# Kernel optimization log

Hardware: AMD Instinct MI355X
Metric: run time of the kernel (lower is better)

## Reference

```python
import jax, jax.numpy as jnp
import numpy as np

B, N, DIM = 2, 2048, 512
H, DH = 8, 64            # heads, dim_head; inner_dim = H*DH = 512 == DIM -> to_out is Identity
BAND = 128               # mask keeps -128 <= j-i <= 127
LN_EPS = 1e-5


def _band_mask(n):
    i = jnp.arange(n)
    d = i[None, :] - i[:, None]          # j - i
    return (d >= -BAND) & (d < BAND)     # [n, n] bool


def setup_inputs() -> dict:
    key = jax.random.key(0)
    k1, k2 = jax.random.split(key, 2)
    x = jax.random.normal(k1, (B, N, DIM), dtype=jnp.float32)
    w_qkv = jax.random.normal(k2, (DIM, 3 * H * DH), dtype=jnp.float32) * (DIM ** -0.5)
    gamma = jnp.ones((DIM,), dtype=jnp.float32)
    beta = jnp.zeros((DIM,), dtype=jnp.float32)
    return {"x": x, "w_qkv": w_qkv, "gamma": gamma, "beta": beta}


def reference(x, w_qkv, gamma, beta):
    # LayerNorm
    mu = jnp.mean(x, axis=-1, keepdims=True)
    var = jnp.mean((x - mu) ** 2, axis=-1, keepdims=True)
    xn = (x - mu) * jax.lax.rsqrt(var + LN_EPS) * gamma + beta

    # qkv projection (no bias); split and reshape to [B, H, N, DH]
    qkv = xn @ w_qkv                                   # [B, N, 3*H*DH]
    q, k, v = jnp.split(qkv, 3, axis=-1)
    to_heads = lambda t: t.reshape(B, N, H, DH).transpose(0, 2, 1, 3)
    q, k, v = to_heads(q), to_heads(k), to_heads(v)

    # NOTE: original forward never applies self.scale -> no scaling here (faithful).
    attn = jnp.einsum('bhnd,bhmd->bhnm', q, k)         # [B, H, N, N]
    attn = jnp.where(_band_mask(N), attn, jnp.float32(-10000.0))
    probs = jax.nn.softmax(attn, axis=-1)
    out = jnp.einsum('bhnm,bhmd->bhnd', probs, v)      # [B, H, N, DH]
    out = out.transpose(0, 2, 1, 3).reshape(B, N, H * DH)
    return out  # to_out is Identity since inner_dim == dim
```

## Files before the change

kernel.cpp:

```cpp
#include <hip/hip_runtime.h>
#include <hip/hip_bf16.h>

#define B_    2
#define N_    2048
#define DIM_  512
#define H_    8
#define DH_   64
#define QKVW  1536
#define BAND_ 128
#define LN_EPS 1e-5f

typedef __attribute__((ext_vector_type(8))) short bf16x8;
typedef __attribute__((ext_vector_type(4))) float f32x4;
typedef __attribute__((ext_vector_type(8))) unsigned short ushort8;

__device__ __forceinline__ float bf2f(unsigned short u) {
    union { unsigned int i; float f; } w; w.i = ((unsigned int)u) << 16; return w.f;
}
__device__ __forceinline__ unsigned short f2bf(float f) {
    __hip_bfloat16 h = __float2bfloat16(f);
    return *reinterpret_cast<unsigned short*>(&h);
}
__device__ __forceinline__ void async_copy16(void* lds, const void* g) {
    __builtin_amdgcn_global_load_lds(
        (const __attribute__((address_space(1))) unsigned int*)g,
        (__attribute__((address_space(3))) unsigned int*)lds, 16, 0, 0);
}

__global__ __launch_bounds__(256) void prep_kernel(const float* __restrict__ x,
                                                   const float* __restrict__ gamma,
                                                   const float* __restrict__ beta,
                                                   const float* __restrict__ W,
                                                   unsigned short* __restrict__ xh,
                                                   unsigned short* __restrict__ xl,
                                                   unsigned short* __restrict__ Bh,
                                                   unsigned short* __restrict__ Bl) {
    __shared__ float T[64][65];
    if (blockIdx.x < 1024) {
        const int row  = blockIdx.x * 4 + (threadIdx.x >> 6);
        const int lane = threadIdx.x & 63;
        const float* xr = x + (size_t)row * DIM_ + lane * 8;
        float4 a = *(const float4*)xr;
        float4 c = *(const float4*)(xr + 4);
        float s  = (a.x + a.y) + (a.z + a.w) + (c.x + c.y) + (c.z + c.w);
        float sq = a.x*a.x + a.y*a.y + a.z*a.z + a.w*a.w
                 + c.x*c.x + c.y*c.y + c.z*c.z + c.w*c.w;
        #pragma unroll
        for (int o = 32; o; o >>= 1) { s += __shfl_xor(s, o); sq += __shfl_xor(sq, o); }
        const float mu  = s * (1.0f / DIM_);
        const float var = sq * (1.0f / DIM_) - mu * mu;
        const float rs  = rsqrtf(var + LN_EPS);
        float4 g0 = *(const float4*)(gamma + lane * 8);
        float4 g1 = *(const float4*)(gamma + lane * 8 + 4);
        float4 b0 = *(const float4*)(beta  + lane * 8);
        float4 b1 = *(const float4*)(beta  + lane * 8 + 4);
        const float fv[8] = {
            (a.x - mu) * rs * g0.x + b0.x, (a.y - mu) * rs * g0.y + b0.y,
            (a.z - mu) * rs * g0.z + b0.z, (a.w - mu) * rs * g0.w + b0.w,
            (c.x - mu) * rs * g1.x + b1.x, (c.y - mu) * rs * g1.y + b1.y,
            (c.z - mu) * rs * g1.z + b1.z, (c.w - mu) * rs * g1.w + b1.w };
        ushort8 h, l;
        #pragma unroll
        for (int j = 0; j < 8; ++j) {
            const unsigned short hv = f2bf(fv[j]);
            h[j] = hv; l[j] = f2bf(fv[j] - bf2f(hv));
        }
        *(ushort8*)(xh + (size_t)row * DIM_ + lane * 8) = h;
        *(ushort8*)(xl + (size_t)row * DIM_ + lane * 8) = l;
    } else {
        const int bx = blockIdx.x - 1024;
        const int n0 = (bx % 24) * 64, k0 = (bx / 24) * 64;
        const int tid = threadIdx.x;
        #pragma unroll
        for (int e = 0; e < 4; ++e) {
            const int lin = e * 256 + tid;
            const int kk = lin >> 4;
            const int n4 = (lin & 15) * 4;
            float4 f = *(const float4*)(W + (size_t)(k0 + kk) * QKVW + n0 + n4);
            T[kk][n4 + 0] = f.x; T[kk][n4 + 1] = f.y;
            T[kk][n4 + 2] = f.z; T[kk][n4 + 3] = f.w;
        }
        __syncthreads();
        #pragma unroll
        for (int e = 0; e < 4; ++e) {
            const int lin = e * 256 + tid;
            const int nn = lin >> 4;
            const int kq = (lin & 15) * 4;
            ushort4 h, l;
            float f;
            f = T[kq + 0][nn]; h.x = f2bf(f); l.x = f2bf(f - bf2f(h.x));
            f = T[kq + 1][nn]; h.y = f2bf(f); l.y = f2bf(f - bf2f(h.y));
            f = T[kq + 2][nn]; h.z = f2bf(f); l.z = f2bf(f - bf2f(h.z));
            f = T[kq + 3][nn]; h.w = f2bf(f); l.w = f2bf(f - bf2f(h.w));
            *(ushort4*)(Bh + (size_t)(n0 + nn) * DIM_ + k0 + kq) = h;
            *(ushort4*)(Bl + (size_t)(n0 + nn) * DIM_ + k0 + kq) = l;
        }
    }
}

__global__ __launch_bounds__(256) void gemm_mfma(const unsigned short* __restrict__ Ah,
                                                 const unsigned short* __restrict__ Al,
                                                 const unsigned short* __restrict__ Bh,
                                                 const unsigned short* __restrict__ Bl,
                                                 unsigned short* __restrict__ Qh,
                                                 unsigned short* __restrict__ Ql,
                                                 unsigned short* __restrict__ Kh,
                                                 unsigned short* __restrict__ Kl,
                                                 unsigned short* __restrict__ Vt) {
    __shared__ __attribute__((aligned(16))) unsigned short sAh[64 * 64],  sAl[64 * 64];
    __shared__ __attribute__((aligned(16))) unsigned short sBh[128 * 64], sBl[128 * 64];
    const int tid  = threadIdx.x;
    const int lane = tid & 63, wave = tid >> 6;
    const int wr = wave >> 1, wc = wave & 1;
    const int lg = lane >> 4, l16 = lane & 15;

    const int bid = blockIdx.x;
    const int sb  = (bid & 7) * 96 + (bid >> 3);
    const int row0 = (sb / 12) * 64;
    const int col0 = (sb % 12) * 128;
    const int part = col0 >> 9;

    f32x4 acc[2][4] = {};

    for (int k0 = 0; k0 < DIM_; k0 += 64) {
        __syncthreads();
        #pragma unroll
        for (int e = 0; e < 2; ++e) {
            const int s0  = e * 256 + wave * 64;
            const int idx = s0 + lane;
            const int r   = idx >> 3;
            const int pb  = idx & 7;
            const int klog = pb ^ (r & 7);
            const size_t ga = (size_t)(row0 + r) * DIM_ + k0 + klog * 8;
            async_copy16(&sAh[s0 * 8], Ah + ga);
            if (part < 2) async_copy16(&sAl[s0 * 8], Al + ga);
        }
        #pragma unroll
        for (int e = 0; e < 4; ++e) {
            const int s0  = e * 256 + wave * 64;
            const int idx = s0 + lane;
            const int r   = idx >> 3;
            const int pb  = idx & 7;
            const int klog = pb ^ (r & 7);
            const size_t gb = (size_t)(col0 + r) * DIM_ + k0 + klog * 8;
            async_copy16(&sBh[s0 * 8], Bh + gb);
            if (part < 2) async_copy16(&sBl[s0 * 8], Bl + gb);
        }
        __syncthreads();

        #pragma unroll
        for (int kh = 0; kh < 2; ++kh) {
            bf16x8 ah[2], bh[4];
            #pragma unroll
            for (int mi = 0; mi < 2; ++mi) {
                const int r = wr * 32 + mi * 16 + l16;
                ah[mi] = *(const bf16x8*)&sAh[r * 64 + (((kh * 4 + lg) ^ (r & 7)) * 8)];
            }
            #pragma unroll
            for (int ni = 0; ni < 4; ++ni) {
                const int r = wc * 64 + ni * 16 + l16;
                bh[ni] = *(const bf16x8*)&sBh[r * 64 + (((kh * 4 + lg) ^ (r & 7)) * 8)];
            }
            if (part < 2) {
                bf16x8 al[2], bl[4];
                #pragma unroll
                for (int mi = 0; mi < 2; ++mi) {
                    const int r = wr * 32 + mi * 16 + l16;
                    al[mi] = *(const bf16x8*)&sAl[r * 64 + (((kh * 4 + lg) ^ (r & 7)) * 8)];
                }
                #pragma unroll
                for (int ni = 0; ni < 4; ++ni) {
                    const int r = wc * 64 + ni * 16 + l16;
                    bl[ni] = *(const bf16x8*)&sBl[r * 64 + (((kh * 4 + lg) ^ (r & 7)) * 8)];
                }
                #pragma unroll
                for (int mi = 0; mi < 2; ++mi)
                    #pragma unroll
                    for (int ni = 0; ni < 4; ++ni) {
                        acc[mi][ni] = __builtin_amdgcn_mfma_f32_16x16x32_bf16(ah[mi], bh[ni], acc[mi][ni], 0, 0, 0);
                        acc[mi][ni] = __builtin_amdgcn_mfma_f32_16x16x32_bf16(al[mi], bh[ni], acc[mi][ni], 0, 0, 0);
                        acc[mi][ni] = __builtin_amdgcn_mfma_f32_16x16x32_bf16(ah[mi], bl[ni], acc[mi][ni], 0, 0, 0);
                    }
            } else {
                #pragma unroll
                for (int mi = 0; mi < 2; ++mi)
                    #pragma unroll
                    for (int ni = 0; ni < 4; ++ni)
                        acc[mi][ni] = __builtin_amdgcn_mfma_f32_16x16x32_bf16(ah[mi], bh[ni], acc[mi][ni], 0, 0, 0);
            }
        }
    }

    const int colbase = col0 + wc * 64;
    const int head = (colbase & 511) >> 6;
    if (part < 2) {
        unsigned short* __restrict__ Ih = (part == 0) ? Qh : Kh;
        unsigned short* __restrict__ Il = (part == 0) ? Ql : Kl;
        #pragma unroll
        for (int mi = 0; mi < 2; ++mi) {
            const int rb = row0 + wr * 32 + mi * 16 + lg * 4;
            const int n  = rb & 2047;
            const size_t tbase = ((size_t)((rb >> 11) * H_ + head) * 32 + (n >> 6)) * 4096;
            #pragma unroll
            for (int ni = 0; ni < 4; ++ni) {
                const int d  = ni * 16 + l16;
                const int k8 = d >> 3;
                #pragma unroll
                for (int rr = 0; rr < 4; ++rr) {
                    const int r = (n & 63) + rr;
                    const size_t off = tbase + r * 64 + ((k8 ^ (r & 7)) * 8) + (d & 7);
                    const float v = acc[mi][ni][rr];
                    const unsigned short hv = f2bf(v);
                    Ih[off] = hv;
                    Il[off] = f2bf(v - bf2f(hv));
                }
            }
        }
    } else {
        #pragma unroll
        for (int mi = 0; mi < 2; ++mi) {
            const int rb = row0 + wr * 32 + mi * 16 + lg * 4;
            const int n  = rb & 2047;
            const size_t cbase = ((size_t)((rb >> 11) * H_ + head) * 32 + (n >> 6)) * 4096;
            const int nr = n & 63;
            #pragma unroll
            for (int ni = 0; ni < 4; ++ni) {
                const int d = ni * 16 + l16;
                const size_t off = cbase + d * 64 + (((nr >> 3) ^ (d & 7)) * 8) + (nr & 7);
                ushort4 pk;
                pk.x = f2bf(acc[mi][ni][0]); pk.y = f2bf(acc[mi][ni][1]);
                pk.z = f2bf(acc[mi][ni][2]); pk.w = f2bf(acc[mi][ni][3]);
                *(ushort4*)&Vt[off] = pk;
            }
        }
    }
}

__global__ __launch_bounds__(256) void attn_mfma(const unsigned short* __restrict__ Qh,
                                                 const unsigned short* __restrict__ Ql,
                                                 const unsigned short* __restrict__ Kh,
                                                 const unsigned short* __restrict__ Kl,
                                                 const unsigned short* __restrict__ Vt,
                                                 float* __restrict__ out) {
    const int bid = blockIdx.x;
    const int sb  = (bid & 7) * 64 + (bid >> 3);
    const int tile = sb & 31;
    const int h    = (sb >> 5) & 7;
    const int b    = sb >> 8;
    const int i0   = tile * 64;
    const int tid  = threadIdx.x;
    const int lane = tid & 63, wave = tid >> 6;
    const int lg   = lane >> 4, l16 = lane & 15;

    __shared__ __attribute__((aligned(16))) unsigned short sKh[4096], sKl[4096], sVt[4096];
    __shared__ __attribute__((aligned(16))) unsigned short sP[4][1024];

    const size_t hb = (size_t)(b * H_ + h) * 32;

    bf16x8 qh[2], ql[2];
    {
        const int r = wave * 16 + l16;
        const size_t tb = (hb + tile) * 4096;
        #pragma unroll
        for (int kh = 0; kh < 2; ++kh) {
            const size_t off = tb + r * 64 + (((kh * 4 + lg) ^ (r & 7)) * 8);
            qh[kh] = *(const bf16x8*)(Qh + off);
            ql[kh] = *(const bf16x8*)(Ql + off);
        }
    }

    float m_run[4], l_run[4];
    f32x4 oacc[4] = {};
    #pragma unroll
    for (int r = 0; r < 4; ++r) { m_run[r] = -1e30f; l_run[r] = 0.0f; }

    #pragma unroll 1
    for (int c = 0; c < 5; ++c) {
        const int jbase = i0 - 128 + c * 64;
        if (jbase + 64 <= 0 || jbase >= N_) continue;
        __syncthreads();
        const size_t kbG = (hb + (jbase >> 6)) * 4096;
        #pragma unroll
        for (int e = 0; e < 6; ++e) {
            const int s0  = e * 256 + wave * 64;
            const int arr = s0 >> 9;
            const int w0  = (s0 & 511) * 8;
            unsigned short* dst = (arr == 0) ? sKh : (arr == 1) ? sKl : sVt;
            const unsigned short* src = (arr == 0) ? Kh : (arr == 1) ? Kl : Vt;
            async_copy16(dst + w0, src + kbG + w0 + lane * 8);
        }
        __syncthreads();

        f32x4 sacc[4] = {};
        #pragma unroll
        for (int kh = 0; kh < 2; ++kh) {
            #pragma unroll
            for (int t = 0; t < 4; ++t) {
                const int r = t * 16 + l16;
                const int off = r * 64 + ((((kh * 4 + lg)) ^ (r & 7)) * 8);
                const bf16x8 kbh = *(const bf16x8*)&sKh[off];
                const bf16x8 kbl = *(const bf16x8*)&sKl[off];
                sacc[t] = __builtin_amdgcn_mfma_f32_16x16x32_bf16(qh[kh], kbh, sacc[t], 0, 0, 0);
                sacc[t] = __builtin_amdgcn_mfma_f32_16x16x32_bf16(ql[kh], kbh, sacc[t], 0, 0, 0);
                sacc[t] = __builtin_amdgcn_mfma_f32_16x16x32_bf16(qh[kh], kbl, sacc[t], 0, 0, 0);
            }
        }

        #pragma unroll
        for (int r = 0; r < 4; ++r) {
            const int i = i0 + wave * 16 + lg * 4 + r;
            float sv[4];
            float mx = -1e30f;
            #pragma unroll
            for (int t = 0; t < 4; ++t) {
                const int j = jbase + t * 16 + l16;
                const int d = j - i;
                const bool ok = (d >= -BAND_) && (d < BAND_);
                sv[t] = ok ? sacc[t][r] : -1e30f;
                mx = fmaxf(mx, sv[t]);
            }
            #pragma unroll
            for (int o = 1; o < 16; o <<= 1) mx = fmaxf(mx, __shfl_xor(mx, o));
            const float m_new = fmaxf(m_run[r], mx);
            const float alpha = __expf(m_run[r] - m_new);
            float p[4], lc = 0.f;
            #pragma unroll
            for (int t = 0; t < 4; ++t) { p[t] = __expf(sv[t] - m_new); lc += p[t]; }
            #pragma unroll
            for (int o = 1; o < 16; o <<= 1) lc += __shfl_xor(lc, o);
            l_run[r] = l_run[r] * alpha + lc;
            m_run[r] = m_new;
            #pragma unroll
            for (int dt = 0; dt < 4; ++dt) oacc[dt][r] *= alpha;
            const int q = lg * 4 + r;
            #pragma unroll
            for (int t = 0; t < 4; ++t) {
                const int k = t * 16 + l16;
                sP[wave][q * 64 + (((k >> 3) ^ (q & 7)) * 8) + (k & 7)] = f2bf(p[t]);
            }
        }

        #pragma unroll
        for (int kh = 0; kh < 2; ++kh) {
            const int poff = l16 * 64 + ((((kh * 4 + lg)) ^ (l16 & 7)) * 8);
            const bf16x8 pa = *(const bf16x8*)&sP[wave][poff];
            #pragma unroll
            for (int dt = 0; dt < 4; ++dt) {
                const int rv = dt * 16 + l16;
                const int voff = rv * 64 + ((((kh * 4 + lg)) ^ (rv & 7)) * 8);
                const bf16x8 vb = *(const bf16x8*)&sVt[voff];
                oacc[dt] = __builtin_amdgcn_mfma_f32_16x16x32_bf16(pa, vb, oacc[dt], 0, 0, 0);
            }
        }
    }

    #pragma unroll
    for (int dt = 0; dt < 4; ++dt)
        #pragma unroll
        for (int r = 0; r < 4; ++r) {
            const int i = i0 + wave * 16 + lg * 4 + r;
            out[((size_t)b * N_ + i) * DIM_ + h * DH_ + dt * 16 + l16] = oacc[dt][r] / l_run[r];
        }
}

extern "C" void kernel_launch(void* const* d_in, const int* in_sizes, int n_in,
                              void* d_out, int out_size, void* d_ws, size_t ws_size,
                              hipStream_t stream) {
    const float* x     = (const float*)d_in[0];
    const float* w     = (const float*)d_in[1];
    const float* gamma = (const float*)d_in[2];
    const float* beta  = (const float*)d_in[3];
    float* out = (float*)d_out;

    const size_t NTOK = (size_t)B_ * N_;
    const size_t IMG  = (size_t)B_ * H_ * 32 * 4096;

    unsigned short* xnh = (unsigned short*)d_ws;
    unsigned short* xnl = xnh + NTOK * DIM_;
    unsigned short* wth = xnl + NTOK * DIM_;
    unsigned short* wtl = wth + (size_t)QKVW * DIM_;
    unsigned short* Qh  = wtl + (size_t)QKVW * DIM_;
    unsigned short* Ql  = Qh + IMG;
    unsigned short* Kh  = Ql + IMG;
    unsigned short* Kl  = Kh + IMG;
    unsigned short* Vt  = Kl + IMG;

    prep_kernel<<<dim3(1024 + 192), dim3(256), 0, stream>>>(x, gamma, beta, w, xnh, xnl, wth, wtl);
    gemm_mfma<<<dim3(768), dim3(256), 0, stream>>>(
        xnh, xnl, wth, wtl, Qh, Ql, Kh, Kl, Vt);
    attn_mfma<<<dim3(512), dim3(256), 0, stream>>>(Qh, Ql, Kh, Kl, Vt, out);
}
```

Measured before the change: 47.08 us.

## Fuse prep, GEMM and attention into one cooperative kernel with grid syncs

Puts the three stages (LayerNorm/weight split, QKV GEMM, banded attention) into one persistent cooperative kernel of 768 blocks with grid-wide barriers between stages, sharing one LDS buffer. The aim is to remove two kernel launch gaps and the tail idling between stages. In exchange it adds grid.sync costs, launch_bounds(256,3) register limits, and per-call host queries of device attributes and occupancy, and it falls back to the three separate kernels when cooperative launch is unavailable.

```diff
diff --git a/kernel.cpp b/kernel.cpp
--- a/kernel.cpp
+++ b/kernel.cpp
@@ -1,5 +1,8 @@
 #include <hip/hip_runtime.h>
 #include <hip/hip_bf16.h>
+#include <hip/hip_cooperative_groups.h>
+
+namespace cg = cooperative_groups;
 
 #define B_    2
 #define N_    2048
@@ -27,17 +30,19 @@
         (__attribute__((address_space(3))) unsigned int*)lds, 16, 0, 0);
 }
 
-__global__ __launch_bounds__(256) void prep_kernel(const float* __restrict__ x,
-                                                   const float* __restrict__ gamma,
-                                                   const float* __restrict__ beta,
-                                                   const float* __restrict__ W,
-                                                   unsigned short* __restrict__ xh,
-                                                   unsigned short* __restrict__ xl,
-                                                   unsigned short* __restrict__ Bh,
-                                                   unsigned short* __restrict__ Bl) {
-    __shared__ float T[64][65];
-    if (blockIdx.x < 1024) {
-        const int row  = blockIdx.x * 4 + (threadIdx.x >> 6);
+
+__device__ void prep_unit(int u,
+                          const float* __restrict__ x,
+                          const float* __restrict__ gamma,
+                          const float* __restrict__ beta,
+                          const float* __restrict__ W,
+                          unsigned short* __restrict__ xh,
+                          unsigned short* __restrict__ xl,
+                          unsigned short* __restrict__ Bh,
+                          unsigned short* __restrict__ Bl,
+                          unsigned char* smem) {
+    if (u < 1024) {
+        const int row  = u * 4 + (threadIdx.x >> 6);
         const int lane = threadIdx.x & 63;
         const float* xr = x + (size_t)row * DIM_ + lane * 8;
         float4 a = *(const float4*)xr;
@@ -68,7 +73,8 @@
         *(ushort8*)(xh + (size_t)row * DIM_ + lane * 8) = h;
         *(ushort8*)(xl + (size_t)row * DIM_ + lane * 8) = l;
     } else {
-        const int bx = blockIdx.x - 1024;
+        float (*T)[65] = (float(*)[65])smem;
+        const int bx = u - 1024;
         const int n0 = (bx % 24) * 64, k0 = (bx / 24) * 64;
         const int tid = threadIdx.x;
         #pragma unroll
@@ -95,26 +101,31 @@
             *(ushort4*)(Bh + (size_t)(n0 + nn) * DIM_ + k0 + kq) = h;
             *(ushort4*)(Bl + (size_t)(n0 + nn) * DIM_ + k0 + kq) = l;
         }
-    }
-}
-
-__global__ __launch_bounds__(256) void gemm_mfma(const unsigned short* __restrict__ Ah,
-                                                 const unsigned short* __restrict__ Al,
-                                                 const unsigned short* __restrict__ Bh,
-                                                 const unsigned short* __restrict__ Bl,
-                                                 unsigned short* __restrict__ Qh,
-                                                 unsigned short* __restrict__ Ql,
-                                                 unsigned short* __restrict__ Kh,
-                                                 unsigned short* __restrict__ Kl,
-                                                 unsigned short* __restrict__ Vt) {
-    __shared__ __attribute__((aligned(16))) unsigned short sAh[64 * 64],  sAl[64 * 64];
-    __shared__ __attribute__((aligned(16))) unsigned short sBh[128 * 64], sBl[128 * 64];
+        __syncthreads();
+    }
+}
+
+__device__ void gemm_body(int bid,
+                          const unsigned short* __restrict__ Ah,
+                          const unsigned short* __restrict__ Al,
+                          const unsigned short* __restrict__ Bh,
+                          const unsigned short* __restrict__ Bl,
+                          unsigned short* __restrict__ Qh,
+                          unsigned short* __restrict__ Ql,
+                          unsigned short* __restrict__ Kh,
+                          unsigned short* __restrict__ Kl,
+                          unsigned short* __restrict__ Vt,
+                          unsigned char* smem) {
+    unsigned short* sAh = (unsigned short*)smem;
+    unsigned short* sAl = sAh + 64 * 64;
+    unsigned short* sBh = sAl + 64 * 64;
+    unsigned short* sBl = sBh + 128 * 64;
+
     const int tid  = threadIdx.x;
     const int lane = tid & 63, wave = tid >> 6;
     const int wr = wave >> 1, wc = wave & 1;
     const int lg = lane >> 4, l16 = lane & 15;
 
-    const int bid = blockIdx.x;
     const int sb  = (bid & 7) * 96 + (bid >> 3);
     const int row0 = (sb / 12) * 64;
     const int col0 = (sb % 12) * 128;
@@ -236,13 +247,19 @@
     }
 }
 
-__global__ __launch_bounds__(256) void attn_mfma(const unsigned short* __restrict__ Qh,
-                                                 const unsigned short* __restrict__ Ql,
-                                                 const unsigned short* __restrict__ Kh,
-                                                 const unsigned short* __restrict__ Kl,
-                                                 const unsigned short* __restrict__ Vt,
-                                                 float* __restrict__ out) {
-    const int bid = blockIdx.x;
+__device__ void attn_body(int bid,
+                          const unsigned short* __restrict__ Qh,
+                          const unsigned short* __restrict__ Ql,
+                          const unsigned short* __restrict__ Kh,
+                          const unsigned short* __restrict__ Kl,
+                          const unsigned short* __restrict__ Vt,
+                          float* __restrict__ out,
+                          unsigned char* smem) {
+    unsigned short* sKh = (unsigned short*)smem;
+    unsigned short* sKl = sKh + 4096;
+    unsigned short* sVt = sKl + 4096;
+    unsigned short* sPb = sVt + 4096;
+
     const int sb  = (bid & 7) * 64 + (bid >> 3);
     const int tile = sb & 31;
     const int h    = (sb >> 5) & 7;
@@ -251,9 +268,7 @@
     const int tid  = threadIdx.x;
     const int lane = tid & 63, wave = tid >> 6;
     const int lg   = lane >> 4, l16 = lane & 15;
-
-    __shared__ __attribute__((aligned(16))) unsigned short sKh[4096], sKl[4096], sVt[4096];
-    __shared__ __attribute__((aligned(16))) unsigned short sP[4][1024];
+    unsigned short* sP = sPb + wave * 1024;
 
     const size_t hb = (size_t)(b * H_ + h) * 32;
 
@@ -336,14 +351,14 @@
             #pragma unroll
             for (int t = 0; t < 4; ++t) {
                 const int k = t * 16 + l16;
-                sP[wave][q * 64 + (((k >> 3) ^ (q & 7)) * 8) + (k & 7)] = f2bf(p[t]);
+                sP[q * 64 + (((k >> 3) ^ (q & 7)) * 8) + (k & 7)] = f2bf(p[t]);
             }
         }
 
         #pragma unroll
         for (int kh = 0; kh < 2; ++kh) {
             const int poff = l16 * 64 + ((((kh * 4 + lg)) ^ (l16 & 7)) * 8);
-            const bf16x8 pa = *(const bf16x8*)&sP[wave][poff];
+            const bf16x8 pa = *(const bf16x8*)&sP[poff];
             #pragma unroll
             for (int dt = 0; dt < 4; ++dt) {
                 const int rv = dt * 16 + l16;
@@ -361,6 +376,56 @@
             const int i = i0 + wave * 16 + lg * 4 + r;
             out[((size_t)b * N_ + i) * DIM_ + h * DH_ + dt * 16 + l16] = oacc[dt][r] / l_run[r];
         }
+}
+
+
+__global__ __launch_bounds__(256) void prep_kernel(const float* x, const float* gamma,
+                                                   const float* beta, const float* W,
+                                                   unsigned short* xh, unsigned short* xl,
+                                                   unsigned short* Bh, unsigned short* Bl) {
+    __shared__ __attribute__((aligned(16))) unsigned char smem[16640];
+    prep_unit(blockIdx.x, x, gamma, beta, W, xh, xl, Bh, Bl, smem);
+}
+
+__global__ __launch_bounds__(256) void gemm_kernel(const unsigned short* Ah, const unsigned short* Al,
+                                                   const unsigned short* Bh, const unsigned short* Bl,
+                                                   unsigned short* Qh, unsigned short* Ql,
+                                                   unsigned short* Kh, unsigned short* Kl,
+                                                   unsigned short* Vt) {
+    __shared__ __attribute__((aligned(16))) unsigned char smem[49152];
+    gemm_body(blockIdx.x, Ah, Al, Bh, Bl, Qh, Ql, Kh, Kl, Vt, smem);
+}
+
+__global__ __launch_bounds__(256) void attn_kernel(const unsigned short* Qh, const unsigned short* Ql,
+                                                   const unsigned short* Kh, const unsigned short* Kl,
+                                                   const unsigned short* Vt, float* out) {
+    __shared__ __attribute__((aligned(16))) unsigned char smem[32768];
+    attn_body(blockIdx.x, Qh, Ql, Kh, Kl, Vt, out, smem);
+}
+
+
+__global__ __launch_bounds__(256, 3) void fused_kernel(const float* x, const float* gamma,
+                                                       const float* beta, const float* W,
+                                                       unsigned short* xh, unsigned short* xl,
+                                                       unsigned short* Bh, unsigned short* Bl,
+                                                       unsigned short* Qh, unsigned short* Ql,
+                                                       unsigned short* Kh, unsigned short* Kl,
+                                                       unsigned short* Vt, float* out) {
+    __shared__ __attribute__((aligned(16))) unsigned char smem[49152];
+    const int bid = blockIdx.x;
+    cg::grid_group grid = cg::this_grid();
+
+    for (int u = bid; u < 1216; u += 768)
+        prep_unit(u, x, gamma, beta, W, xh, xl, Bh, Bl, smem);
+    __threadfence();
+    grid.sync();
+
+    gemm_body(bid, xh, xl, Bh, Bl, Qh, Ql, Kh, Kl, Vt, smem);
+    __threadfence();
+    grid.sync();
+
+    if (bid < 512)
+        attn_body(bid, Qh, Ql, Kh, Kl, Vt, out, smem);
 }
 
 extern "C" void kernel_launch(void* const* d_in, const int* in_sizes, int n_in,
@@ -385,8 +450,22 @@
     unsigned short* Kl  = Kh + IMG;
     unsigned short* Vt  = Kl + IMG;
 
-    prep_kernel<<<dim3(1024 + 192), dim3(256), 0, stream>>>(x, gamma, beta, w, xnh, xnl, wth, wtl);
-    gemm_mfma<<<dim3(768), dim3(256), 0, stream>>>(
-        xnh, xnl, wth, wtl, Qh, Ql, Kh, Kl, Vt);
-    attn_mfma<<<dim3(512), dim3(256), 0, stream>>>(Qh, Ql, Kh, Kl, Vt, out);
-}
+    int coop = 0, nCU = 0, maxB = 0;
+    hipDeviceGetAttribute(&coop, hipDeviceAttributeCooperativeLaunch, 0);
+    hipDeviceGetAttribute(&nCU, hipDeviceAttributeMultiprocessorCount, 0);
+    hipOccupancyMaxActiveBlocksPerMultiprocessor(&maxB, fused_kernel, 256, 0);
+
+    if (coop && (long)maxB * nCU >= 768) {
+        void* args[] = { (void*)&x, (void*)&gamma, (void*)&beta, (void*)&w,
+                         (void*)&xnh, (void*)&xnl, (void*)&wth, (void*)&wtl,
+                         (void*)&Qh, (void*)&Ql, (void*)&Kh, (void*)&Kl,
+                         (void*)&Vt, (void*)&out };
+        if (hipLaunchCooperativeKernel((const void*)fused_kernel, dim3(768), dim3(256),
+                                       args, 0, stream) == hipSuccess)
+            return;
+    }
+
+    prep_kernel<<<dim3(1216), dim3(256), 0, stream>>>(x, gamma, beta, w, xnh, xnl, wth, wtl);
+    gemm_kernel<<<dim3(768), dim3(256), 0, stream>>>(xnh, xnl, wth, wtl, Qh, Ql, Kh, Kl, Vt);
+    attn_kernel<<<dim3(512), dim3(256), 0, stream>>>(Qh, Ql, Kh, Kl, Vt, out);
+}
```

After: 74.35 us. 57.9% more time.
